# Kernel tuning notes

Hardware: AMD Instinct MI355X
Metric: run time of the kernel (lower is better)

The kernel has to match this reference:

```python
import jax, jax.numpy as jnp
import numpy as np

B, N, M, D, H = 8, 2048, 2048, 512, 8


def setup_inputs() -> dict:
    key = jax.random.key(0)
    ks = jax.random.split(key, 12)
    std = D ** (-0.5)
    inp = {
        "k": jax.random.normal(ks[0], (B, N, D), jnp.float32),
        "v": jax.random.normal(ks[1], (B, N, D), jnp.float32),
        "q": jax.random.normal(ks[2], (B, M, D), jnp.float32),
        # per-head projections, stacked over the head axis: [H, D, D]
        "Wk": jax.random.normal(ks[3], (H, D, D), jnp.float32) * std,
        "bk": jax.random.normal(ks[4], (H, D), jnp.float32) * 0.01,
        "Wv": jax.random.normal(ks[5], (H, D, D), jnp.float32) * std,
        "bv": jax.random.normal(ks[6], (H, D), jnp.float32) * 0.01,
        "Wq": jax.random.normal(ks[7], (H, D, D), jnp.float32) * std,
        "bq": jax.random.normal(ks[8], (H, D), jnp.float32) * 0.01,
        # final linear: input ordering is (hidden_dim, head) flattened -> H*D
        "Wo": jax.random.normal(ks[9], (H * D, D), jnp.float32) * (H * D) ** (-0.5),
        "bo": jax.random.normal(ks[10], (D,), jnp.float32) * 0.01,
    }
    return inp


def reference(k, v, q, Wk, bk, Wv, bv, Wq, bq, Wo, bo):
    # Per-head linear projections (torch loops over heads; here batched over h).
    # nn.Linear computes x @ W.T + b; Wk here stores W.T directly as [H, D, D].
    k_ = jnp.einsum("bnd,hde->bhne", k, Wk) + bk[None, :, None, :]  # [B,H,N,D]
    v_ = jnp.einsum("bnd,hde->bhne", v, Wv) + bv[None, :, None, :]  # [B,H,N,D]
    q_ = jnp.einsum("bmd,hde->bhme", q, Wq) + bq[None, :, None, :]  # [B,H,M,D]

    scale = D ** 0.5
    scores = jnp.einsum("bhmd,bhnd->bhmn", q_, k_) / scale  # [B,H,M,N]
    weights = jax.nn.softmax(scores, axis=-1)
    out = jnp.einsum("bhmn,bhnd->bhmd", weights, v_)  # [B,H,M,D]

    # torch: stack(outs, dim=-1) -> [B,M,D,H], then view -> [B,M,D*H]
    outs = jnp.transpose(out, (0, 2, 3, 1)).reshape(B, M, D * H)
    # matching flatten order (d-major, h-minor) requires Wo rows ordered d*H+h;
    # setup generates Wo random so any consistent ordering is faithful.
    rep = outs @ Wo + bo  # [B,M,D]
    return rep
```

## Files before the change

### kernel.cpp

```cpp
#include <hip/hip_runtime.h>
#include <hip/hip_bf16.h>
#include <cstdint>
#include <cstddef>

typedef __bf16 bf16x8 __attribute__((ext_vector_type(8)));
typedef __bf16 bf16x4 __attribute__((ext_vector_type(4)));
typedef float floatx4 __attribute__((ext_vector_type(4)));

#define MFMA16(a, b, c) __builtin_amdgcn_mfma_f32_16x16x32_bf16((a), (b), (c), 0, 0, 0)

__device__ __forceinline__ void load_lds16(const __bf16* g, __bf16* l) {
  __builtin_amdgcn_global_load_lds(
      (const __attribute__((address_space(1))) uint32_t*)(g),
      (__attribute__((address_space(3))) uint32_t*)(l), 16, 0, 0);
}

#define BAR_LGKM()                                        \
  do {                                                    \
    asm volatile("s_waitcnt lgkmcnt(0)" ::: "memory");    \
    __builtin_amdgcn_s_barrier();                         \
    __builtin_amdgcn_sched_barrier(0);                    \
  } while (0)

__device__ __forceinline__ int xcd_swizzle(int orig, int nwg) {
  int q = nwg >> 3, r = nwg & 7;
  int xcd = orig & 7, local = orig >> 3;
  return (xcd < r) ? xcd * (q + 1) + local : r * (q + 1) + (xcd - r) * q + local;
}

__global__ __launch_bounds__(256) void tw_t(const float* __restrict__ W,
                                            __bf16* __restrict__ Wt, float scale) {
  __shared__ float tile[64][65];
  int h = blockIdx.z, d0 = blockIdx.y * 64, e0 = blockIdx.x * 64;
  int tx = threadIdx.x & 15, ty = threadIdx.x >> 4;
  const float* src = W + ((size_t)h * 512 + d0) * 512 + e0;
#pragma unroll
  for (int j = 0; j < 4; ++j) {
    int dd = ty + j * 16;
    float4 f = *(const float4*)&src[(size_t)dd * 512 + tx * 4];
    tile[dd][tx * 4 + 0] = f.x; tile[dd][tx * 4 + 1] = f.y;
    tile[dd][tx * 4 + 2] = f.z; tile[dd][tx * 4 + 3] = f.w;
  }
  __syncthreads();
  __bf16* dst = Wt + ((size_t)h * 512 + e0) * 512 + d0;
#pragma unroll
  for (int j = 0; j < 4; ++j) {
    int ee = ty + j * 16;
    bf16x4 v;
#pragma unroll
    for (int x = 0; x < 4; ++x) v[x] = (__bf16)(tile[tx * 4 + x][ee] * scale);
    *(bf16x4*)&dst[(size_t)ee * 512 + tx * 4] = v;
  }
}

__global__ __launch_bounds__(256) void wo_t(const float* __restrict__ Wo,
                                            __bf16* __restrict__ Wot) {
  __shared__ float tile[64][65];
  int h = blockIdx.z, d0 = blockIdx.y * 64, e0 = blockIdx.x * 64;
  int tx = threadIdx.x & 15, ty = threadIdx.x >> 4;
#pragma unroll
  for (int j = 0; j < 4; ++j) {
    int dd = ty + j * 16;
    float4 f = *(const float4*)&Wo[(size_t)((d0 + dd) * 8 + h) * 512 + e0 + tx * 4];
    tile[dd][tx * 4 + 0] = f.x; tile[dd][tx * 4 + 1] = f.y;
    tile[dd][tx * 4 + 2] = f.z; tile[dd][tx * 4 + 3] = f.w;
  }
  __syncthreads();
#pragma unroll
  for (int j = 0; j < 4; ++j) {
    int ee = ty + j * 16;
    bf16x4 v;
#pragma unroll
    for (int x = 0; x < 4; ++x) v[x] = (__bf16)tile[tx * 4 + x][ee];
    *(bf16x4*)&Wot[(size_t)(e0 + ee) * 4096 + h * 512 + d0 + tx * 4] = v;
  }
}

__global__ __launch_bounds__(256) void cvt_bf16x3(const float* __restrict__ in0,
                                                  const float* __restrict__ in1,
                                                  const float* __restrict__ in2,
                                                  __bf16* __restrict__ out0,
                                                  __bf16* __restrict__ out1,
                                                  __bf16* __restrict__ out2,
                                                  int n8) {
  int i = blockIdx.x * 256 + threadIdx.x;
  if (i >= n8) return;
  const float* in = (blockIdx.y == 0) ? in0 : (blockIdx.y == 1) ? in1 : in2;
  __bf16* out = (blockIdx.y == 0) ? out0 : (blockIdx.y == 1) ? out1 : out2;
  float4 f0 = *(const float4*)&in[(size_t)i * 8];
  float4 f1 = *(const float4*)&in[(size_t)i * 8 + 4];
  bf16x8 v;
  v[0] = (__bf16)f0.x; v[1] = (__bf16)f0.y; v[2] = (__bf16)f0.z; v[3] = (__bf16)f0.w;
  v[4] = (__bf16)f1.x; v[5] = (__bf16)f1.y; v[6] = (__bf16)f1.z; v[7] = (__bf16)f1.w;
  *(bf16x8*)&out[(size_t)i * 8] = v;
}

template <int EPI>
__global__ __launch_bounds__(256) void gemm_bt(const __bf16* __restrict__ A,
                                               const __bf16* __restrict__ Bt,
                                               const float* __restrict__ bias,
                                               void* __restrict__ Cout,
                                               int N, int K, float bscale) {
  __shared__ __align__(16) __bf16 sA[128][72];
  __shared__ __align__(16) __bf16 sB[128][72];
  const int tid = threadIdx.x;
  const int lane = tid & 63;
  const int wave = tid >> 6;
  const int lr = lane & 15;
  const int lq = lane >> 4;
  const int wm = (wave >> 1) * 64;
  const int wn = (wave & 1) * 64;
  const int bx = blockIdx.x, by = blockIdx.y;
  const int srow = tid >> 3;
  const int scol = (tid & 7) << 3;

  const floatx4 z4 = {0.f, 0.f, 0.f, 0.f};
  floatx4 acc[4][4];
#pragma unroll
  for (int i = 0; i < 4; ++i)
#pragma unroll
    for (int j = 0; j < 4; ++j) acc[i][j] = z4;

  const size_t abase = (size_t)(by * 128) * K;
  const size_t bbase = (size_t)(bx * 128) * K;

  for (int k0 = 0; k0 < K; k0 += 64) {
#pragma unroll
    for (int p = 0; p < 4; ++p) {
      int row = p * 32 + srow;
      *(bf16x8*)&sA[row][scol] = *(const bf16x8*)&A[abase + (size_t)row * K + k0 + scol];
      *(bf16x8*)&sB[row][scol] = *(const bf16x8*)&Bt[bbase + (size_t)row * K + k0 + scol];
    }
    __syncthreads();
#pragma unroll
    for (int ks = 0; ks < 2; ++ks) {
      bf16x8 af[4], bfr[4];
#pragma unroll
      for (int mt = 0; mt < 4; ++mt)
        af[mt] = *(const bf16x8*)&sA[wm + mt * 16 + lr][ks * 32 + lq * 8];
#pragma unroll
      for (int nt = 0; nt < 4; ++nt)
        bfr[nt] = *(const bf16x8*)&sB[wn + nt * 16 + lr][ks * 32 + lq * 8];
#pragma unroll
      for (int mt = 0; mt < 4; ++mt)
#pragma unroll
        for (int nt = 0; nt < 4; ++nt) acc[mt][nt] = MFMA16(af[mt], bfr[nt], acc[mt][nt]);
    }
    __syncthreads();
  }

#pragma unroll
  for (int mt = 0; mt < 4; ++mt) {
#pragma unroll
    for (int nt = 0; nt < 4; ++nt) {
      int col = bx * 128 + wn + nt * 16 + lr;
      int row0 = by * 128 + wm + mt * 16 + lq * 4;
      float bcol = bias[col] * bscale;
      if (EPI == 0) {
        __bf16* dst = (__bf16*)Cout;
        int h = col >> 9, e = col & 511;
#pragma unroll
        for (int r = 0; r < 4; ++r) {
          int row = row0 + r;
          int b = row >> 11, m = row & 2047;
          dst[((size_t)((b << 3) | h) * 2048 + m) * 512 + e] = (__bf16)(acc[mt][nt][r] + bcol);
        }
      } else if (EPI == 1) {
        __bf16* dst = (__bf16*)Cout;
        int h = col >> 9, e = col & 511;
        int b = row0 >> 11, n = row0 & 2047;
        bf16x4 pk;
#pragma unroll
        for (int r = 0; r < 4; ++r) pk[r] = (__bf16)(acc[mt][nt][r] + bcol);
        *(bf16x4*)&dst[((size_t)((b << 3) | h) * 512 + e) * 2048 + n] = pk;
      } else {
        float* dst = (float*)Cout;
#pragma unroll
        for (int r = 0; r < 4; ++r) {
          int row = row0 + r;
          dst[(size_t)row * N + col] = acc[mt][nt][r] + bcol;
        }
      }
    }
  }
}

__global__ __launch_bounds__(512, 2) void attn_kernel(const __bf16* __restrict__ Qp,
                                                      const __bf16* __restrict__ Kp,
                                                      const __bf16* __restrict__ Vt,
                                                      __bf16* __restrict__ Outs) {
  __shared__ __align__(16) __bf16 kls[2][32 * 512];
  __shared__ __align__(16) __bf16 vls[2][512 * 32];
  __shared__ __align__(16) __bf16 pls[128 * 40];
  __shared__ __align__(16) floatx4 sx[2][8][64];
  __shared__ __align__(16) float l_red[128];
  const int tid = threadIdx.x;
  const int lane = tid & 63;
  const int wave = tid >> 6;
  const int lr = lane & 15;
  const int lq = lane >> 4;
  const int blk = xcd_swizzle(blockIdx.x, gridDim.x);
  const int bh = blk >> 4;
  const int mblk = blk & 15;
  const int rp = (wave & 3) * 2;
  const int dh = wave >> 2;
  const int fg = rp + dh;
  const int e0 = wave * 64;
  const int mbase = mblk * 128;
  const __bf16* Qb = Qp + (size_t)bh * (2048 * 512);
  const __bf16* Kb = Kp + (size_t)bh * (2048 * 512);
  const __bf16* Vb = Vt + (size_t)bh * (512 * 2048);

  int gK[4], gV[4];
#pragma unroll
  for (int i = 0; i < 4; ++i) {
    int q = i * 512 + tid;
    int rK = q >> 6;
    gK[i] = rK * 512 + ((q & 63) ^ (rK & 7)) * 8;
    int eV = q >> 2;
    gV[i] = eV * 2048 + ((q & 3) ^ (eV & 3)) * 8;
  }

  bf16x8 qf[2][8];
#pragma unroll
  for (int ks = 0; ks < 8; ++ks) {
    qf[0][ks] = *(const bf16x8*)&Qb[(size_t)(mbase + fg * 16 + lr) * 512 +
                                    dh * 256 + ks * 32 + lq * 8];
    qf[1][ks] = *(const bf16x8*)&Qb[(size_t)(mbase + (rp + (dh ^ 1)) * 16 + lr) * 512 +
                                    dh * 256 + ks * 32 + lq * 8];
  }

  const floatx4 z4 = {0.f, 0.f, 0.f, 0.f};
  floatx4 o[8][4];
#pragma unroll
  for (int mt = 0; mt < 8; ++mt)
#pragma unroll
    for (int et = 0; et < 4; ++et) o[mt][et] = z4;
  float lsum[4] = {0.f, 0.f, 0.f, 0.f};

#pragma unroll
  for (int i = 0; i < 4; ++i) {
    load_lds16(Kb + gK[i], &kls[0][i * 4096 + wave * 512]);
    load_lds16(Vb + gV[i], &vls[0][i * 4096 + wave * 512]);
  }
  __syncthreads();

  for (int t = 0; t < 64; ++t) {
    const int cur = t & 1;
    if (t < 63) {
      const __bf16* kg = Kb + (size_t)(t + 1) * (32 * 512);
      const __bf16* vg = Vb + (t + 1) * 32;
#pragma unroll
      for (int i = 0; i < 4; ++i) {
        load_lds16(kg + gK[i], &kls[cur ^ 1][i * 4096 + wave * 512]);
        load_lds16(vg + gV[i], &vls[cur ^ 1][i * 4096 + wave * 512]);
      }
    }
    floatx4 sm0 = z4, sm1 = z4, sp0 = z4, sp1 = z4;
    const __bf16* kc = kls[cur];
#pragma unroll
    for (int ks = 0; ks < 8; ++ks) {
      int cidx = ((dh * 32 + ks * 4 + lq) ^ (lr & 7)) * 8;
      bf16x8 k0 = *(const bf16x8*)&kc[lr * 512 + cidx];
      bf16x8 k1 = *(const bf16x8*)&kc[(16 + lr) * 512 + cidx];
      sm0 = MFMA16(qf[0][ks], k0, sm0);
      sm1 = MFMA16(qf[0][ks], k1, sm1);
      sp0 = MFMA16(qf[1][ks], k0, sp0);
      sp1 = MFMA16(qf[1][ks], k1, sp1);
    }
    sx[0][wave][lane] = sp0;
    sx[1][wave][lane] = sp1;
    BAR_LGKM();
    {
      floatx4 q0 = sx[0][wave ^ 4][lane];
      floatx4 q1 = sx[1][wave ^ 4][lane];
#pragma unroll
      for (int r = 0; r < 4; ++r) {
        float p0 = __expf(sm0[r] + q0[r]);
        float p1 = __expf(sm1[r] + q1[r]);
        lsum[r] += p0 + p1;
        pls[(fg * 16 + lq * 4 + r) * 40 + lr] = (__bf16)p0;
        pls[(fg * 16 + lq * 4 + r) * 40 + 16 + lr] = (__bf16)p1;
      }
    }
    BAR_LGKM();
    {
      const __bf16* vc = vls[cur];
      bf16x8 vf[4];
#pragma unroll
      for (int et = 0; et < 4; ++et) {
        int e = e0 + et * 16 + lr;
        vf[et] = *(const bf16x8*)&vc[e * 32 + ((lq ^ (e & 3)) * 8)];
      }
#pragma unroll
      for (int mt = 0; mt < 8; ++mt) {
        bf16x8 pf = *(const bf16x8*)&pls[(mt * 16 + lr) * 40 + lq * 8];
#pragma unroll
        for (int et = 0; et < 4; ++et) o[mt][et] = MFMA16(pf, vf[et], o[mt][et]);
      }
    }
    __syncthreads();
  }

#pragma unroll
  for (int r = 0; r < 4; ++r) {
    float s = lsum[r];
    s += __shfl_xor(s, 1);
    s += __shfl_xor(s, 2);
    s += __shfl_xor(s, 4);
    s += __shfl_xor(s, 8);
    lsum[r] = s;
  }
  if (lr == 0) {
#pragma unroll
    for (int r = 0; r < 4; ++r) l_red[fg * 16 + lq * 4 + r] = lsum[r];
  }
  __syncthreads();

  int b = bh >> 3, h = bh & 7;
#pragma unroll
  for (int mt = 0; mt < 8; ++mt) {
    float4 lv = *(const float4*)&l_red[mt * 16 + lq * 4];
    float invr[4] = {1.0f / lv.x, 1.0f / lv.y, 1.0f / lv.z, 1.0f / lv.w};
    size_t rowbase = ((size_t)b * 2048 + mbase + mt * 16 + lq * 4) * 4096 + h * 512 + e0;
#pragma unroll
    for (int et = 0; et < 4; ++et)
#pragma unroll
      for (int r = 0; r < 4; ++r)
        Outs[rowbase + (size_t)r * 4096 + et * 16 + lr] = (__bf16)(o[mt][et][r] * invr[r]);
  }
}

extern "C" void kernel_launch(void* const* d_in, const int* in_sizes, int n_in,
                              void* d_out, int out_size, void* d_ws, size_t ws_size,
                              hipStream_t stream) {
  (void)in_sizes; (void)n_in; (void)out_size;
  const float* kin = (const float*)d_in[0];
  const float* vin = (const float*)d_in[1];
  const float* qin = (const float*)d_in[2];
  const float* Wk  = (const float*)d_in[3];
  const float* bk  = (const float*)d_in[4];
  const float* Wv  = (const float*)d_in[5];
  const float* bv  = (const float*)d_in[6];
  const float* Wq  = (const float*)d_in[7];
  const float* bq  = (const float*)d_in[8];
  const float* Wo  = (const float*)d_in[9];
  const float* bo  = (const float*)d_in[10];
  float* out = (float*)d_out;
  char* ws = (char*)d_ws;

  const float scale = 0.044194173824159216f;

  const size_t SZ_W = (size_t)4096 * 512 * 2;
  const size_t SZ_B = (size_t)8 * 2048 * 512 * 2;
  const size_t FIXED = 4 * SZ_W;

  int nb = 1;
  if (ws_size >= FIXED + 8 * 4 * SZ_B) nb = 8;
  else if (ws_size >= FIXED + 4 * 4 * SZ_B) nb = 4;
  else if (ws_size >= FIXED + 2 * 4 * SZ_B) nb = 2;

  __bf16* Wkt = (__bf16*)(ws);
  __bf16* Wvt = (__bf16*)(ws + SZ_W);
  __bf16* Wqt = (__bf16*)(ws + 2 * SZ_W);
  __bf16* Wot = (__bf16*)(ws + 3 * SZ_W);
  char* chunkbase = ws + FIXED;
  __bf16* kproj = (__bf16*)(chunkbase);
  __bf16* qproj = (__bf16*)(chunkbase + (size_t)nb * SZ_B);
  __bf16* vt    = (__bf16*)(chunkbase + (size_t)nb * 2 * SZ_B);
  __bf16* outs  = (__bf16*)(chunkbase + (size_t)nb * 3 * SZ_B);

  tw_t<<<dim3(8, 8, 8), dim3(256), 0, stream>>>(Wk, Wkt, 1.0f);
  tw_t<<<dim3(8, 8, 8), dim3(256), 0, stream>>>(Wv, Wvt, 1.0f);
  tw_t<<<dim3(8, 8, 8), dim3(256), 0, stream>>>(Wq, Wqt, scale);
  wo_t<<<dim3(8, 8, 8), dim3(256), 0, stream>>>(Wo, Wot);

  for (int b0 = 0; b0 < 8; b0 += nb) {
    const float* kc = kin + (size_t)b0 * 2048 * 512;
    const float* vc = vin + (size_t)b0 * 2048 * 512;
    const float* qc = qin + (size_t)b0 * 2048 * 512;
    const size_t chunk_els = (size_t)nb * 2048 * 512;
    __bf16* kb16 = outs;
    __bf16* qb16 = outs + chunk_els;
    __bf16* vb16 = outs + 2 * chunk_els;
    int n8 = (int)(chunk_els / 8);
    int cvgrid = (n8 + 255) / 256;
    cvt_bf16x3<<<dim3(cvgrid, 3), dim3(256), 0, stream>>>(kc, qc, vc, kb16, qb16, vb16, n8);
    gemm_bt<0><<<dim3(32, nb * 16), dim3(256), 0, stream>>>(kb16, Wkt, bk, (void*)kproj, 4096, 512, 1.0f);
    gemm_bt<0><<<dim3(32, nb * 16), dim3(256), 0, stream>>>(qb16, Wqt, bq, (void*)qproj, 4096, 512, scale);
    gemm_bt<1><<<dim3(32, nb * 16), dim3(256), 0, stream>>>(vb16, Wvt, bv, (void*)vt, 4096, 512, 1.0f);
    attn_kernel<<<dim3(nb * 128), dim3(512), 0, stream>>>(qproj, kproj, vt, outs);
    gemm_bt<2><<<dim3(4, nb * 16), dim3(256), 0, stream>>>(
        outs, Wot, bo, (void*)(out + (size_t)b0 * 2048 * 512), 512, 4096, 1.0f);
  }
}
```

Measured before the change: 1.526 ms.

## Load V directly from global in attention, merge weight-prep and projection launches

The attention kernel stops staging V tiles through LDS with async global-to-LDS loads. Each wave now reads its V fragments straight from global memory at the top of every iteration, which frees LDS and removes that copy. Separately, the four weight-transpose launches are merged into one grid, and the three projection GEMMs become one launch with a z-dimension. This cuts launch overhead and lets the projections share the GPU. The risk is that the direct global V loads in attention expose latency that LDS double-buffering used to hide.

```diff
diff --git a/kernel.cpp b/kernel.cpp
--- a/kernel.cpp
+++ b/kernel.cpp
@@ -28,51 +28,59 @@
   return (xcd < r) ? xcd * (q + 1) + local : r * (q + 1) + (xcd - r) * q + local;
 }
 
-__global__ __launch_bounds__(256) void tw_t(const float* __restrict__ W,
-                                            __bf16* __restrict__ Wt, float scale) {
+__global__ __launch_bounds__(256) void wt_all(const float* __restrict__ Wk,
+                                              const float* __restrict__ Wv,
+                                              const float* __restrict__ Wq,
+                                              const float* __restrict__ Wo,
+                                              __bf16* __restrict__ Wkt,
+                                              __bf16* __restrict__ Wvt,
+                                              __bf16* __restrict__ Wqt,
+                                              __bf16* __restrict__ Wot,
+                                              float qscale) {
   __shared__ float tile[64][65];
-  int h = blockIdx.z, d0 = blockIdx.y * 64, e0 = blockIdx.x * 64;
+  int z = blockIdx.z;
+  int which = z >> 3, h = z & 7;
+  int d0 = blockIdx.y * 64, e0 = blockIdx.x * 64;
   int tx = threadIdx.x & 15, ty = threadIdx.x >> 4;
-  const float* src = W + ((size_t)h * 512 + d0) * 512 + e0;
-#pragma unroll
-  for (int j = 0; j < 4; ++j) {
-    int dd = ty + j * 16;
-    float4 f = *(const float4*)&src[(size_t)dd * 512 + tx * 4];
-    tile[dd][tx * 4 + 0] = f.x; tile[dd][tx * 4 + 1] = f.y;
-    tile[dd][tx * 4 + 2] = f.z; tile[dd][tx * 4 + 3] = f.w;
-  }
-  __syncthreads();
-  __bf16* dst = Wt + ((size_t)h * 512 + e0) * 512 + d0;
-#pragma unroll
-  for (int j = 0; j < 4; ++j) {
-    int ee = ty + j * 16;
-    bf16x4 v;
-#pragma unroll
-    for (int x = 0; x < 4; ++x) v[x] = (__bf16)(tile[tx * 4 + x][ee] * scale);
-    *(bf16x4*)&dst[(size_t)ee * 512 + tx * 4] = v;
-  }
-}
-
-__global__ __launch_bounds__(256) void wo_t(const float* __restrict__ Wo,
-                                            __bf16* __restrict__ Wot) {
-  __shared__ float tile[64][65];
-  int h = blockIdx.z, d0 = blockIdx.y * 64, e0 = blockIdx.x * 64;
-  int tx = threadIdx.x & 15, ty = threadIdx.x >> 4;
-#pragma unroll
-  for (int j = 0; j < 4; ++j) {
-    int dd = ty + j * 16;
-    float4 f = *(const float4*)&Wo[(size_t)((d0 + dd) * 8 + h) * 512 + e0 + tx * 4];
-    tile[dd][tx * 4 + 0] = f.x; tile[dd][tx * 4 + 1] = f.y;
-    tile[dd][tx * 4 + 2] = f.z; tile[dd][tx * 4 + 3] = f.w;
-  }
-  __syncthreads();
-#pragma unroll
-  for (int j = 0; j < 4; ++j) {
-    int ee = ty + j * 16;
-    bf16x4 v;
-#pragma unroll
-    for (int x = 0; x < 4; ++x) v[x] = (__bf16)tile[tx * 4 + x][ee];
-    *(bf16x4*)&Wot[(size_t)(e0 + ee) * 4096 + h * 512 + d0 + tx * 4] = v;
+  if (which < 3) {
+    const float* W = (which == 0) ? Wk : (which == 1) ? Wv : Wq;
+    __bf16* Wt = (which == 0) ? Wkt : (which == 1) ? Wvt : Wqt;
+    float scale = (which == 2) ? qscale : 1.0f;
+    const float* src = W + ((size_t)h * 512 + d0) * 512 + e0;
+#pragma unroll
+    for (int j = 0; j < 4; ++j) {
+      int dd = ty + j * 16;
+      float4 f = *(const float4*)&src[(size_t)dd * 512 + tx * 4];
+      tile[dd][tx * 4 + 0] = f.x; tile[dd][tx * 4 + 1] = f.y;
+      tile[dd][tx * 4 + 2] = f.z; tile[dd][tx * 4 + 3] = f.w;
+    }
+    __syncthreads();
+    __bf16* dst = Wt + ((size_t)h * 512 + e0) * 512 + d0;
+#pragma unroll
+    for (int j = 0; j < 4; ++j) {
+      int ee = ty + j * 16;
+      bf16x4 v;
+#pragma unroll
+      for (int x = 0; x < 4; ++x) v[x] = (__bf16)(tile[tx * 4 + x][ee] * scale);
+      *(bf16x4*)&dst[(size_t)ee * 512 + tx * 4] = v;
+    }
+  } else {
+#pragma unroll
+    for (int j = 0; j < 4; ++j) {
+      int dd = ty + j * 16;
+      float4 f = *(const float4*)&Wo[(size_t)((d0 + dd) * 8 + h) * 512 + e0 + tx * 4];
+      tile[dd][tx * 4 + 0] = f.x; tile[dd][tx * 4 + 1] = f.y;
+      tile[dd][tx * 4 + 2] = f.z; tile[dd][tx * 4 + 3] = f.w;
+    }
+    __syncthreads();
+#pragma unroll
+    for (int j = 0; j < 4; ++j) {
+      int ee = ty + j * 16;
+      bf16x4 v;
+#pragma unroll
+      for (int x = 0; x < 4; ++x) v[x] = (__bf16)tile[tx * 4 + x][ee];
+      *(bf16x4*)&Wot[(size_t)(e0 + ee) * 4096 + h * 512 + d0 + tx * 4] = v;
+    }
   }
 }
 
@@ -95,12 +103,112 @@
   *(bf16x8*)&out[(size_t)i * 8] = v;
 }
 
-template <int EPI>
-__global__ __launch_bounds__(256) void gemm_bt(const __bf16* __restrict__ A,
-                                               const __bf16* __restrict__ Bt,
-                                               const float* __restrict__ bias,
-                                               void* __restrict__ Cout,
-                                               int N, int K, float bscale) {
+__device__ __forceinline__ void gemm_core(const __bf16* __restrict__ A,
+                                          const __bf16* __restrict__ Bt,
+                                          __bf16 (*sA)[72], __bf16 (*sB)[72],
+                                          floatx4 (&acc)[4][4],
+                                          size_t abase, size_t bbase, int K,
+                                          int wm, int wn, int lr, int lq,
+                                          int srow, int scol) {
+  for (int k0 = 0; k0 < K; k0 += 64) {
+#pragma unroll
+    for (int p = 0; p < 4; ++p) {
+      int row = p * 32 + srow;
+      *(bf16x8*)&sA[row][scol] = *(const bf16x8*)&A[abase + (size_t)row * K + k0 + scol];
+      *(bf16x8*)&sB[row][scol] = *(const bf16x8*)&Bt[bbase + (size_t)row * K + k0 + scol];
+    }
+    __syncthreads();
+#pragma unroll
+    for (int ks = 0; ks < 2; ++ks) {
+      bf16x8 af[4], bfr[4];
+#pragma unroll
+      for (int mt = 0; mt < 4; ++mt)
+        af[mt] = *(const bf16x8*)&sA[wm + mt * 16 + lr][ks * 32 + lq * 8];
+#pragma unroll
+      for (int nt = 0; nt < 4; ++nt)
+        bfr[nt] = *(const bf16x8*)&sB[wn + nt * 16 + lr][ks * 32 + lq * 8];
+#pragma unroll
+      for (int mt = 0; mt < 4; ++mt)
+#pragma unroll
+        for (int nt = 0; nt < 4; ++nt) acc[mt][nt] = MFMA16(af[mt], bfr[nt], acc[mt][nt]);
+    }
+    __syncthreads();
+  }
+}
+
+__global__ __launch_bounds__(256) void gemm_proj(const __bf16* __restrict__ kb16,
+                                                 const __bf16* __restrict__ qb16,
+                                                 const __bf16* __restrict__ vb16,
+                                                 const __bf16* __restrict__ Wkt,
+                                                 const __bf16* __restrict__ Wqt,
+                                                 const __bf16* __restrict__ Wvt,
+                                                 const float* __restrict__ bk,
+                                                 const float* __restrict__ bq,
+                                                 const float* __restrict__ bv,
+                                                 __bf16* __restrict__ kproj,
+                                                 __bf16* __restrict__ qproj,
+                                                 __bf16* __restrict__ vt,
+                                                 float qscale) {
+  __shared__ __align__(16) __bf16 sA[128][72];
+  __shared__ __align__(16) __bf16 sB[128][72];
+  const int tid = threadIdx.x;
+  const int lane = tid & 63;
+  const int wave = tid >> 6;
+  const int lr = lane & 15;
+  const int lq = lane >> 4;
+  const int wm = (wave >> 1) * 64;
+  const int wn = (wave & 1) * 64;
+  const int bx = blockIdx.x, by = blockIdx.y, z = blockIdx.z;
+  const int srow = tid >> 3;
+  const int scol = (tid & 7) << 3;
+  const int K = 512;
+
+  const __bf16* A = (z == 0) ? kb16 : (z == 1) ? qb16 : vb16;
+  const __bf16* Bt = (z == 0) ? Wkt : (z == 1) ? Wqt : Wvt;
+  const float* bias = (z == 0) ? bk : (z == 1) ? bq : bv;
+  const float bscale = (z == 1) ? qscale : 1.0f;
+
+  const floatx4 z4 = {0.f, 0.f, 0.f, 0.f};
+  floatx4 acc[4][4];
+#pragma unroll
+  for (int i = 0; i < 4; ++i)
+#pragma unroll
+    for (int j = 0; j < 4; ++j) acc[i][j] = z4;
+
+  gemm_core(A, Bt, sA, sB, acc, (size_t)(by * 128) * K, (size_t)(bx * 128) * K,
+            K, wm, wn, lr, lq, srow, scol);
+
+#pragma unroll
+  for (int mt = 0; mt < 4; ++mt) {
+#pragma unroll
+    for (int nt = 0; nt < 4; ++nt) {
+      int col = bx * 128 + wn + nt * 16 + lr;
+      int row0 = by * 128 + wm + mt * 16 + lq * 4;
+      float bcol = bias[col] * bscale;
+      int h = col >> 9, e = col & 511;
+      if (z < 2) {
+        __bf16* dst = (z == 0) ? kproj : qproj;
+#pragma unroll
+        for (int r = 0; r < 4; ++r) {
+          int row = row0 + r;
+          int b = row >> 11, m = row & 2047;
+          dst[((size_t)((b << 3) | h) * 2048 + m) * 512 + e] = (__bf16)(acc[mt][nt][r] + bcol);
+        }
+      } else {
+        int b = row0 >> 11, n = row0 & 2047;
+        bf16x4 pk;
+#pragma unroll
+        for (int r = 0; r < 4; ++r) pk[r] = (__bf16)(acc[mt][nt][r] + bcol);
+        *(bf16x4*)&vt[((size_t)((b << 3) | h) * 512 + e) * 2048 + n] = pk;
+      }
+    }
+  }
+}
+
+__global__ __launch_bounds__(256) void gemm_out(const __bf16* __restrict__ A,
+                                                const __bf16* __restrict__ Bt,
+                                                const float* __restrict__ bias,
+                                                float* __restrict__ Cout, int N) {
   __shared__ __align__(16) __bf16 sA[128][72];
   __shared__ __align__(16) __bf16 sB[128][72];
   const int tid = threadIdx.x;
@@ -113,6 +221,7 @@
   const int bx = blockIdx.x, by = blockIdx.y;
   const int srow = tid >> 3;
   const int scol = (tid & 7) << 3;
+  const int K = 4096;
 
   const floatx4 z4 = {0.f, 0.f, 0.f, 0.f};
   floatx4 acc[4][4];
@@ -121,33 +230,8 @@
 #pragma unroll
     for (int j = 0; j < 4; ++j) acc[i][j] = z4;
 
-  const size_t abase = (size_t)(by * 128) * K;
-  const size_t bbase = (size_t)(bx * 128) * K;
-
-  for (int k0 = 0; k0 < K; k0 += 64) {
-#pragma unroll
-    for (int p = 0; p < 4; ++p) {
-      int row = p * 32 + srow;
-      *(bf16x8*)&sA[row][scol] = *(const bf16x8*)&A[abase + (size_t)row * K + k0 + scol];
-      *(bf16x8*)&sB[row][scol] = *(const bf16x8*)&Bt[bbase + (size_t)row * K + k0 + scol];
-    }
-    __syncthreads();
-#pragma unroll
-    for (int ks = 0; ks < 2; ++ks) {
-      bf16x8 af[4], bfr[4];
-#pragma unroll
-      for (int mt = 0; mt < 4; ++mt)
-        af[mt] = *(const bf16x8*)&sA[wm + mt * 16 + lr][ks * 32 + lq * 8];
-#pragma unroll
-      for (int nt = 0; nt < 4; ++nt)
-        bfr[nt] = *(const bf16x8*)&sB[wn + nt * 16 + lr][ks * 32 + lq * 8];
-#pragma unroll
-      for (int mt = 0; mt < 4; ++mt)
-#pragma unroll
-        for (int nt = 0; nt < 4; ++nt) acc[mt][nt] = MFMA16(af[mt], bfr[nt], acc[mt][nt]);
-    }
-    __syncthreads();
-  }
+  gemm_core(A, Bt, sA, sB, acc, (size_t)(by * 128) * K, (size_t)(bx * 128) * K,
+            K, wm, wn, lr, lq, srow, scol);
 
 #pragma unroll
   for (int mt = 0; mt < 4; ++mt) {
@@ -155,31 +239,11 @@
     for (int nt = 0; nt < 4; ++nt) {
       int col = bx * 128 + wn + nt * 16 + lr;
       int row0 = by * 128 + wm + mt * 16 + lq * 4;
-      float bcol = bias[col] * bscale;
-      if (EPI == 0) {
-        __bf16* dst = (__bf16*)Cout;
-        int h = col >> 9, e = col & 511;
-#pragma unroll
-        for (int r = 0; r < 4; ++r) {
-          int row = row0 + r;
-          int b = row >> 11, m = row & 2047;
-          dst[((size_t)((b << 3) | h) * 2048 + m) * 512 + e] = (__bf16)(acc[mt][nt][r] + bcol);
-        }
-      } else if (EPI == 1) {
-        __bf16* dst = (__bf16*)Cout;
-        int h = col >> 9, e = col & 511;
-        int b = row0 >> 11, n = row0 & 2047;
-        bf16x4 pk;
-#pragma unroll
-        for (int r = 0; r < 4; ++r) pk[r] = (__bf16)(acc[mt][nt][r] + bcol);
-        *(bf16x4*)&dst[((size_t)((b << 3) | h) * 512 + e) * 2048 + n] = pk;
-      } else {
-        float* dst = (float*)Cout;
-#pragma unroll
-        for (int r = 0; r < 4; ++r) {
-          int row = row0 + r;
-          dst[(size_t)row * N + col] = acc[mt][nt][r] + bcol;
-        }
+      float bcol = bias[col];
+#pragma unroll
+      for (int r = 0; r < 4; ++r) {
+        int row = row0 + r;
+        Cout[(size_t)row * N + col] = acc[mt][nt][r] + bcol;
       }
     }
   }
@@ -190,7 +254,6 @@
                                                       const __bf16* __restrict__ Vt,
                                                       __bf16* __restrict__ Outs) {
   __shared__ __align__(16) __bf16 kls[2][32 * 512];
-  __shared__ __align__(16) __bf16 vls[2][512 * 32];
   __shared__ __align__(16) __bf16 pls[128 * 40];
   __shared__ __align__(16) floatx4 sx[2][8][64];
   __shared__ __align__(16) float l_red[128];
@@ -211,15 +274,17 @@
   const __bf16* Kb = Kp + (size_t)bh * (2048 * 512);
   const __bf16* Vb = Vt + (size_t)bh * (512 * 2048);
 
-  int gK[4], gV[4];
+  int gK[4];
 #pragma unroll
   for (int i = 0; i < 4; ++i) {
     int q = i * 512 + tid;
     int rK = q >> 6;
     gK[i] = rK * 512 + ((q & 63) ^ (rK & 7)) * 8;
-    int eV = q >> 2;
-    gV[i] = eV * 2048 + ((q & 3) ^ (eV & 3)) * 8;
-  }
+  }
+  const __bf16* vbase[4];
+#pragma unroll
+  for (int et = 0; et < 4; ++et)
+    vbase[et] = Vb + (size_t)(e0 + et * 16 + lr) * 2048 + lq * 8;
 
   bf16x8 qf[2][8];
 #pragma unroll
@@ -239,22 +304,19 @@
   float lsum[4] = {0.f, 0.f, 0.f, 0.f};
 
 #pragma unroll
-  for (int i = 0; i < 4; ++i) {
-    load_lds16(Kb + gK[i], &kls[0][i * 4096 + wave * 512]);
-    load_lds16(Vb + gV[i], &vls[0][i * 4096 + wave * 512]);
-  }
+  for (int i = 0; i < 4; ++i) load_lds16(Kb + gK[i], &kls[0][i * 4096 + wave * 512]);
   __syncthreads();
 
   for (int t = 0; t < 64; ++t) {
     const int cur = t & 1;
+    bf16x8 vf[4];
+#pragma unroll
+    for (int et = 0; et < 4; ++et) vf[et] = *(const bf16x8*)(vbase[et] + t * 32);
     if (t < 63) {
       const __bf16* kg = Kb + (size_t)(t + 1) * (32 * 512);
-      const __bf16* vg = Vb + (t + 1) * 32;
-#pragma unroll
-      for (int i = 0; i < 4; ++i) {
+#pragma unroll
+      for (int i = 0; i < 4; ++i)
         load_lds16(kg + gK[i], &kls[cur ^ 1][i * 4096 + wave * 512]);
-        load_lds16(vg + gV[i], &vls[cur ^ 1][i * 4096 + wave * 512]);
-      }
     }
     floatx4 sm0 = z4, sm1 = z4, sp0 = z4, sp1 = z4;
     const __bf16* kc = kls[cur];
@@ -285,13 +347,6 @@
     }
     BAR_LGKM();
     {
-      const __bf16* vc = vls[cur];
-      bf16x8 vf[4];
-#pragma unroll
-      for (int et = 0; et < 4; ++et) {
-        int e = e0 + et * 16 + lr;
-        vf[et] = *(const bf16x8*)&vc[e * 32 + ((lq ^ (e & 3)) * 8)];
-      }
 #pragma unroll
       for (int mt = 0; mt < 8; ++mt) {
         bf16x8 pf = *(const bf16x8*)&pls[(mt * 16 + lr) * 40 + lq * 8];
@@ -370,10 +425,7 @@
   __bf16* vt    = (__bf16*)(chunkbase + (size_t)nb * 2 * SZ_B);
   __bf16* outs  = (__bf16*)(chunkbase + (size_t)nb * 3 * SZ_B);
 
-  tw_t<<<dim3(8, 8, 8), dim3(256), 0, stream>>>(Wk, Wkt, 1.0f);
-  tw_t<<<dim3(8, 8, 8), dim3(256), 0, stream>>>(Wv, Wvt, 1.0f);
-  tw_t<<<dim3(8, 8, 8), dim3(256), 0, stream>>>(Wq, Wqt, scale);
-  wo_t<<<dim3(8, 8, 8), dim3(256), 0, stream>>>(Wo, Wot);
+  wt_all<<<dim3(8, 8, 32), dim3(256), 0, stream>>>(Wk, Wv, Wq, Wo, Wkt, Wvt, Wqt, Wot, scale);
 
   for (int b0 = 0; b0 < 8; b0 += nb) {
     const float* kc = kin + (size_t)b0 * 2048 * 512;
@@ -386,11 +438,10 @@
     int n8 = (int)(chunk_els / 8);
     int cvgrid = (n8 + 255) / 256;
     cvt_bf16x3<<<dim3(cvgrid, 3), dim3(256), 0, stream>>>(kc, qc, vc, kb16, qb16, vb16, n8);
-    gemm_bt<0><<<dim3(32, nb * 16), dim3(256), 0, stream>>>(kb16, Wkt, bk, (void*)kproj, 4096, 512, 1.0f);
-    gemm_bt<0><<<dim3(32, nb * 16), dim3(256), 0, stream>>>(qb16, Wqt, bq, (void*)qproj, 4096, 512, scale);
-    gemm_bt<1><<<dim3(32, nb * 16), dim3(256), 0, stream>>>(vb16, Wvt, bv, (void*)vt, 4096, 512, 1.0f);
+    gemm_proj<<<dim3(32, nb * 16, 3), dim3(256), 0, stream>>>(
+        kb16, qb16, vb16, Wkt, Wqt, Wvt, bk, bq, bv, kproj, qproj, vt, scale);
     attn_kernel<<<dim3(nb * 128), dim3(512), 0, stream>>>(qproj, kproj, vt, outs);
-    gemm_bt<2><<<dim3(4, nb * 16), dim3(256), 0, stream>>>(
-        outs, Wot, bo, (void*)(out + (size_t)b0 * 2048 * 512), 512, 4096, 1.0f);
-  }
-}
+    gemm_out<<<dim3(4, nb * 16), dim3(256), 0, stream>>>(
+        outs, Wot, bo, out + (size_t)b0 * 2048 * 512, 512);
+  }
+}
```

Result: faster. 1.422 ms (-6.8%).
